# Performance work log

Hardware: AMD Instinct MI355X
Metric: run time of the kernel (lower is better)

The kernel has to match this reference:

```python
import jax, jax.numpy as jnp
import numpy as np

BN_EPS = 1e-5

def _bn_eval(x, gamma, beta):
    # Fresh torch BatchNorm1d in eval mode: running_mean=0, running_var=1
    return x * (gamma / jnp.sqrt(1.0 + BN_EPS)) + beta

def setup_inputs() -> dict:
    key = jax.random.key(0)
    ks = jax.random.split(key, 10)
    Q, K, H, W, D = 64, 128, 24, 8, 128
    L = H * W            # seq_len = 192
    FF = 2048            # dim_feedforward
    q_feat = jax.random.normal(ks[0], (Q, H, W, D), dtype=jnp.float32)
    g_feat = jax.random.normal(ks[1], (K, H, W, D), dtype=jnp.float32)
    se = jax.random.normal(ks[2], (L, L), dtype=jnp.float32)
    score_embed = (se + se.T).reshape(1, 1, L, L)
    s = 1.0 / np.sqrt(D)
    fc0_w = jax.random.uniform(ks[3], (D, D), jnp.float32, -s, s)
    fc0_b = jax.random.uniform(ks[4], (D,), jnp.float32, -s, s)
    s2 = 1.0 / np.sqrt(L)
    fc2_w = jax.random.uniform(ks[5], (FF, L), jnp.float32, -s2, s2)
    fc2_b = jax.random.uniform(ks[6], (FF,), jnp.float32, -s2, s2)
    s3 = 1.0 / np.sqrt(FF)
    fc3_w = jax.random.uniform(ks[7], (1, FF), jnp.float32, -s3, s3)
    fc3_b = jax.random.uniform(ks[8], (1,), jnp.float32, -s3, s3)
    bn1_g = jnp.ones((1,)); bn1_b = jnp.zeros((1,))
    bn2_g = jnp.ones((FF,)) + 0.1 * jax.random.normal(ks[9], (FF,), jnp.float32)
    bn2_b = jnp.zeros((FF,))
    bn3_g = jnp.ones((1,)); bn3_b = jnp.zeros((1,))
    return dict(q_feat=q_feat, g_feat=g_feat, score_embed=score_embed,
                fc0_w=fc0_w, fc0_b=fc0_b, fc2_w=fc2_w, fc2_b=fc2_b,
                fc3_w=fc3_w, fc3_b=fc3_b, bn1_g=bn1_g, bn1_b=bn1_b,
                bn2_g=bn2_g, bn2_b=bn2_b, bn3_g=bn3_g, bn3_b=bn3_b)

def reference(q_feat, g_feat, score_embed, fc0_w, fc0_b, fc2_w, fc2_b,
              fc3_w, fc3_b, bn1_g, bn1_b, bn2_g, bn2_b, bn3_g, bn3_b):
    Q = q_feat.shape[0]
    K = g_feat.shape[0]
    D = q_feat.shape[-1]
    L = score_embed.shape[-1]  # seq_len
    tgt = q_feat.reshape(Q, L, D)
    mem = g_feat.reshape(K, L, D)
    query = tgt @ fc0_w.T + fc0_b      # [Q, L, D]
    key_ = mem @ fc0_w.T + fc0_b       # [K, L, D]
    # [Q, K, L(s), L(t)] score, modulated by broadcast sigmoid bias
    score = jnp.einsum('qtd,ksd->qkst', query, key_) * jax.nn.sigmoid(score_embed)
    score = score.reshape(Q * K, L, L)
    # max over s and over t, concatenated per pair -> [QK, 2L]
    score = jnp.concatenate([score.max(axis=1), score.max(axis=2)], axis=-1)
    score = score.reshape(-1, L)       # [2*QK, L]
    score = _bn_eval(score, bn1_g, bn1_b)
    score = score @ fc2_w.T + fc2_b    # [2*QK, FF]
    score = _bn_eval(score, bn2_g, bn2_b)
    score = jax.nn.relu(score)
    score = score @ fc3_w.T + fc3_b    # [2*QK, 1]
    score = score.reshape(-1, 2).sum(axis=-1, keepdims=True)  # [QK, 1]
    score = _bn_eval(score, bn3_g, bn3_b)
    return score.reshape(Q, K)
```

## Files before the change

kernel.cpp:

```cpp
#include <hip/hip_runtime.h>
#include <hip/hip_fp16.h>

#define LL 192
#define FF 2048

typedef __attribute__((__ext_vector_type__(8)))  __bf16 bf16x8;
typedef __attribute__((__ext_vector_type__(4)))  __bf16 bf16x4;
typedef __attribute__((__ext_vector_type__(4)))  float  f32x4;
typedef __attribute__((__ext_vector_type__(2)))  _Float16 f16x2;

#define MFMA16(a, b, c) __builtin_amdgcn_mfma_f32_16x16x32_bf16((a), (b), (c), 0, 0, 0)


#define ASYNC_LDS16(g, l)                                        \
    __builtin_amdgcn_global_load_lds(                            \
        (const __attribute__((address_space(1))) void*)(g),      \
        (__attribute__((address_space(3))) void*)(l), 16, 0, 0)

template<int CTL>
__device__ __forceinline__ unsigned dppu(unsigned x) {
    return (unsigned)__builtin_amdgcn_mov_dpp((int)x, CTL, 0xF, 0xF, true);
}
__device__ __forceinline__ unsigned pkrtz_u(float a, float b) {
    return __builtin_bit_cast(unsigned, __builtin_amdgcn_cvt_pkrtz(a, b));
}
__device__ __forceinline__ unsigned hmax2u(unsigned a, unsigned b) {
    unsigned r;
    asm("v_pk_max_f16 %0, %1, %2" : "=v"(r) : "v"(a), "v"(b));
    return r;
}

__launch_bounds__(256, 2)
__global__ void proj_prep_kernel(const float* __restrict__ qf_in,
                                 const float* __restrict__ gf_in,
                                 const float* __restrict__ fc0w,
                                 const float* __restrict__ fc0b,
                                 const float* __restrict__ se,
                                 const float* __restrict__ fc2w,
                                 const float* __restrict__ fc2b,
                                 const float* __restrict__ bn2g,
                                 const float* __restrict__ bn2b,
                                 const float* __restrict__ fc3w,
                                 __bf16* __restrict__ kfragA,
                                 __bf16* __restrict__ qfrag16,
                                 float* __restrict__ sig32,
                                 __bf16* __restrict__ fc2w_bf,
                                 float* __restrict__ h2,
                                 float* __restrict__ bb2,
                                 float* __restrict__ f3)
{
    int bx = blockIdx.x, tid = threadIdx.x;
    if (bx >= 1152) {
        int i0 = (bx - 1152) * 256 + tid;
        const int stride = 160 * 256;
        const float c1 = rsqrtf(1.f + 1e-5f);
        for (int i = i0; i < LL * LL; i += stride) {
            int r = i & 3, lane = (i >> 2) & 63, tile = i >> 8;
            int jt = tile % 12, st = tile / 12;
            int s = st * 16 + (lane >> 4) * 4 + r;
            int t = jt * 16 + (lane & 15);
            sig32[i] = 1.f / (1.f + __expf(-se[s * 192 + t]));
        }
        for (int i = i0; i < FF * LL; i += stride)
            fc2w_bf[i] = (__bf16)fc2w[i];
        for (int i = i0; i < FF; i += stride) {
            float h = bn2g[i] * c1;
            h2[i]  = h;
            bb2[i] = fc2b[i] * h + bn2b[i];
            f3[i]  = fc3w[i];
        }
        return;
    }
    __shared__ __bf16 Xs[32][136];
    __shared__ __bf16 Ws[128][136];
    __shared__ __bf16 Os[4096];
    const float* src = (bx < 384) ? (qf_in + (size_t)bx * (32 * 128))
                                  : (gf_in + (size_t)(bx - 384) * (32 * 128));
#pragma unroll
    for (int it = 0; it < 4; ++it) {
        int e = (it * 256 + tid) * 4;
        int r = e >> 7, c = e & 127;
        float4 v = *reinterpret_cast<const float4*>(src + e);
        bf16x4 xv;
        xv[0] = (__bf16)v.x; xv[1] = (__bf16)v.y;
        xv[2] = (__bf16)v.z; xv[3] = (__bf16)v.w;
        *reinterpret_cast<bf16x4*>(&Xs[r][c]) = xv;
    }
#pragma unroll
    for (int it = 0; it < 16; ++it) {
        int e = (it * 256 + tid) * 4;
        int r = e >> 7, c = e & 127;
        float4 v = *reinterpret_cast<const float4*>(fc0w + e);
        bf16x4 xv;
        xv[0] = (__bf16)v.x; xv[1] = (__bf16)v.y;
        xv[2] = (__bf16)v.z; xv[3] = (__bf16)v.w;
        *reinterpret_cast<bf16x4*>(&Ws[r][c]) = xv;
    }
    __syncthreads();

    int wv = tid >> 6, lane = tid & 63, quad = lane >> 4, l16 = lane & 15;
    int n0 = wv * 32;
    f32x4 acc[2][2];
#pragma unroll
    for (int m = 0; m < 2; ++m)
#pragma unroll
        for (int n = 0; n < 2; ++n) acc[m][n] = (f32x4){0.f, 0.f, 0.f, 0.f};
#pragma unroll
    for (int ks = 0; ks < 4; ++ks) {
        bf16x8 a0 = *reinterpret_cast<const bf16x8*>(&Xs[l16][ks * 32 + quad * 8]);
        bf16x8 a1 = *reinterpret_cast<const bf16x8*>(&Xs[16 + l16][ks * 32 + quad * 8]);
        bf16x8 b0 = *reinterpret_cast<const bf16x8*>(&Ws[n0 + l16][ks * 32 + quad * 8]);
        bf16x8 b1 = *reinterpret_cast<const bf16x8*>(&Ws[n0 + 16 + l16][ks * 32 + quad * 8]);
        acc[0][0] = MFMA16(a0, b0, acc[0][0]);
        acc[0][1] = MFMA16(a0, b1, acc[0][1]);
        acc[1][0] = MFMA16(a1, b0, acc[1][0]);
        acc[1][1] = MFMA16(a1, b1, acc[1][1]);
    }
#pragma unroll
    for (int mt = 0; mt < 2; ++mt)
#pragma unroll
        for (int nt = 0; nt < 2; ++nt) {
            int d = n0 + nt * 16 + l16;
            float bv = fc0b[d];
            int abase = mt * 2048 + (d >> 5) * 512 + ((d >> 3) & 3) * 128 + (d & 7);
#pragma unroll
            for (int r = 0; r < 4; ++r)
                Os[abase + (quad * 4 + r) * 8] = (__bf16)(acc[mt][nt][r] + bv);
        }
    __syncthreads();

    int row0 = bx * 32;
    __bf16* dst;
    if (bx < 384) {
        int qi = row0 / 192, tg0 = (row0 % 192) >> 4;
        dst = qfrag16 + qi * 24576 + tg0 * 2048;
    } else {
        int rk0 = row0 - 12288;
        int ki = rk0 / 192, sg0 = (rk0 % 192) >> 4;
        dst = kfragA + ki * 24576 + sg0 * 2048;
    }
#pragma unroll
    for (int it = 0; it < 2; ++it) {
        int e = (it * 256 + tid) * 8;
        *reinterpret_cast<bf16x8*>(dst + e) =
            *reinterpret_cast<const bf16x8*>(&Os[e]);
    }
}

__launch_bounds__(256, 1)
__global__ void score_kernel(const __bf16* __restrict__ kfragA,
                             const __bf16* __restrict__ qfrag16,
                             const float* __restrict__ sig32,
                             const float* __restrict__ bn1g,
                             const float* __restrict__ bn1b,
                             __bf16* __restrict__ Sred)
{
    __shared__ __bf16 Abuf[8192];
    __shared__ unsigned rowP[2][16][98];

    int tid = threadIdx.x;
    int q0 = (blockIdx.x & 31) * 2;
    int kbase = (blockIdx.x >> 5) << 2;
    int w = tid >> 6, lane = tid & 63, quad = lane >> 4, l16 = lane & 15;
    const float g1c = bn1g[0] * rsqrtf(1.f + 1e-5f);
    const float b1v = bn1b[0];

    bf16x8 Bf[2][3][4];
#pragma unroll
    for (int p = 0; p < 2; ++p) {
        const __bf16* qb = qfrag16 + (size_t)(q0 + p) * 24576 + lane * 8;
#pragma unroll
        for (int j = 0; j < 3; ++j)
#pragma unroll
            for (int ks = 0; ks < 4; ++ks)
                Bf[p][j][ks] = *reinterpret_cast<const bf16x8*>(
                    qb + ((3 * w + j) * 4 + ks) * 512);
    }

#pragma unroll 1
    for (int kk = 0; kk < 4; ++kk) {
        int kidx = kbase + kk;
        const __bf16* kp = kfragA + (size_t)kidx * 24576;
        float cm[2][3];
#pragma unroll
        for (int p = 0; p < 2; ++p)
#pragma unroll
            for (int j = 0; j < 3; ++j) cm[p][j] = -3.0e38f;

#pragma unroll 1
        for (int h = 0; h < 3; ++h) {
#pragma unroll
            for (int it = 0; it < 4; ++it)
                ASYNC_LDS16(kp + 8192 * h + (it * 256 + tid) * 8,
                            &Abuf[(it * 256 + (tid & 192)) * 8]);
            __syncthreads();

#pragma unroll
            for (int lsc = 0; lsc < 2; ++lsc) {
                f32x4 acc[2][2][3];
#pragma unroll
                for (int p = 0; p < 2; ++p)
#pragma unroll
                    for (int i = 0; i < 2; ++i)
#pragma unroll
                        for (int j = 0; j < 3; ++j)
                            acc[p][i][j] = (f32x4){0.f, 0.f, 0.f, 0.f};

#pragma unroll
                for (int ks = 0; ks < 4; ++ks) {
                    bf16x8 a0 = *reinterpret_cast<const bf16x8*>(
                        &Abuf[((lsc * 2 + 0) * 4 + ks) * 512 + lane * 8]);
                    bf16x8 a1 = *reinterpret_cast<const bf16x8*>(
                        &Abuf[((lsc * 2 + 1) * 4 + ks) * 512 + lane * 8]);
#pragma unroll
                    for (int j = 0; j < 3; ++j) {
                        acc[0][0][j] = MFMA16(a0, Bf[0][j][ks], acc[0][0][j]);
                        acc[0][1][j] = MFMA16(a1, Bf[0][j][ks], acc[0][1][j]);
                        acc[1][0][j] = MFMA16(a0, Bf[1][j][ks], acc[1][0][j]);
                        acc[1][1][j] = MFMA16(a1, Bf[1][j][ks], acc[1][1][j]);
                    }
                }

#pragma unroll
                for (int i = 0; i < 2; ++i) {
                    int stile = 4 * h + lsc * 2 + i;
                    const float* sp = sig32 +
                        ((size_t)(stile * 12 + 3 * w) * 64 + lane) * 4;
                    f32x4 s0 = *reinterpret_cast<const f32x4*>(sp);
                    f32x4 s1 = *reinterpret_cast<const f32x4*>(sp + 256);
                    f32x4 s2 = *reinterpret_cast<const f32x4*>(sp + 512);
#pragma unroll
                    for (int p = 0; p < 2; ++p) {
                        f32x4 v0 = acc[p][i][0] * s0;
                        f32x4 v1 = acc[p][i][1] * s1;
                        f32x4 v2 = acc[p][i][2] * s2;
                        cm[p][0] = fmaxf(fmaxf(cm[p][0], fmaxf(v0[0], v0[1])),
                                         fmaxf(v0[2], v0[3]));
                        cm[p][1] = fmaxf(fmaxf(cm[p][1], fmaxf(v1[0], v1[1])),
                                         fmaxf(v1[2], v1[3]));
                        cm[p][2] = fmaxf(fmaxf(cm[p][2], fmaxf(v2[0], v2[1])),
                                         fmaxf(v2[2], v2[3]));
                        unsigned h01 = pkrtz_u(
                            fmaxf(fmaxf(v0[0], v1[0]), v2[0]),
                            fmaxf(fmaxf(v0[1], v1[1]), v2[1]));
                        unsigned h23 = pkrtz_u(
                            fmaxf(fmaxf(v0[2], v1[2]), v2[2]),
                            fmaxf(fmaxf(v0[3], v1[3]), v2[3]));
                        h01 = hmax2u(h01, dppu<0xB1>(h01));
                        h01 = hmax2u(h01, dppu<0x4E>(h01));
                        h23 = hmax2u(h23, dppu<0xB1>(h23));
                        h23 = hmax2u(h23, dppu<0x4E>(h23));
                        if ((l16 & 3) == 0) {
                            int rp = stile * 8 + quad * 2;
                            rowP[p][(l16 >> 2) * 4 + w][rp]     = h01;
                            rowP[p][(l16 >> 2) * 4 + w][rp + 1] = h23;
                        }
                    }
                }
            }
            __syncthreads();
        }

#pragma unroll
        for (int p = 0; p < 2; ++p) {
            size_t ob = (size_t)((q0 + p) * 128 + kidx) * 384;
            float v0 = cm[p][0], v1 = cm[p][1], v2 = cm[p][2];
            v0 = fmaxf(v0, __shfl_xor(v0, 16, 64));
            v0 = fmaxf(v0, __shfl_xor(v0, 32, 64));
            v1 = fmaxf(v1, __shfl_xor(v1, 16, 64));
            v1 = fmaxf(v1, __shfl_xor(v1, 32, 64));
            v2 = fmaxf(v2, __shfl_xor(v2, 16, 64));
            v2 = fmaxf(v2, __shfl_xor(v2, 32, 64));
            if (quad == 0) {
                Sred[ob + (3 * w + 0) * 16 + l16] = (__bf16)(v0 * g1c + b1v);
                Sred[ob + (3 * w + 1) * 16 + l16] = (__bf16)(v1 * g1c + b1v);
                Sred[ob + (3 * w + 2) * 16 + l16] = (__bf16)(v2 * g1c + b1v);
            }
        }

        if (tid < 96) {
#pragma unroll
            for (int p = 0; p < 2; ++p) {
                size_t ob = (size_t)((q0 + p) * 128 + kidx) * 384;
                unsigned m = rowP[p][0][tid];
#pragma unroll
                for (int c = 1; c < 16; ++c)
                    m = hmax2u(m, rowP[p][c][tid]);
                __half2 hm = __builtin_bit_cast(__half2, m);
                float lo = __low2float(hm), hi = __high2float(hm);
                unsigned two =
                    (unsigned)__builtin_bit_cast(unsigned short,
                        (__bf16)(lo * g1c + b1v)) |
                    ((unsigned)__builtin_bit_cast(unsigned short,
                        (__bf16)(hi * g1c + b1v)) << 16);
                *reinterpret_cast<unsigned*>(&Sred[ob + 192 + 2 * tid]) = two;
            }
        }
    }
}

__launch_bounds__(512, 1)
__global__ void mlp_kernel(const __bf16* __restrict__ Sred,
                           const __bf16* __restrict__ fc2w_bf,
                           const float* __restrict__ h2,
                           const float* __restrict__ bb2,
                           const float* __restrict__ f3,
                           const float* __restrict__ fc3b,
                           const float* __restrict__ bn3g,
                           const float* __restrict__ bn3b,
                           float* __restrict__ out)
{
    __shared__ __bf16 As[64][200];
    __shared__ float  psum_lds[8][64];
    int bx = blockIdx.x, tid = threadIdx.x;
    const __bf16* asrc = Sred + (size_t)bx * (64 * 192);
#pragma unroll
    for (int it = 0; it < 3; ++it) {
        int e = (it * 512 + tid) * 8;
        int r = e / 192, c = e - r * 192;
        *reinterpret_cast<bf16x8*>(&As[r][c]) =
            *reinterpret_cast<const bf16x8*>(asrc + e);
    }
    __syncthreads();

    int wv = tid >> 6, lane = tid & 63, quad = lane >> 4, l16 = lane & 15;
    bf16x8 af[4][6];
#pragma unroll
    for (int m = 0; m < 4; ++m)
#pragma unroll
        for (int kk = 0; kk < 6; ++kk)
            af[m][kk] = *reinterpret_cast<const bf16x8*>(
                &As[m * 16 + l16][kk * 32 + quad * 8]);

    float ps[4][4] = {{0.f,0.f,0.f,0.f},{0.f,0.f,0.f,0.f},
                      {0.f,0.f,0.f,0.f},{0.f,0.f,0.f,0.f}};
    for (int nt = 0; nt < 16; ++nt) {
        int n0 = wv * 256 + nt * 16;
        f32x4 acc[4];
#pragma unroll
        for (int m = 0; m < 4; ++m) acc[m] = (f32x4){0.f, 0.f, 0.f, 0.f};
        const __bf16* bp = fc2w_bf + (size_t)(n0 + l16) * 192 + quad * 8;
#pragma unroll
        for (int kk = 0; kk < 6; ++kk) {
            bf16x8 b = *reinterpret_cast<const bf16x8*>(bp + kk * 32);
#pragma unroll
            for (int m = 0; m < 4; ++m) acc[m] = MFMA16(af[m][kk], b, acc[m]);
        }
        int n = n0 + l16;
        float hh = h2[n], bb = bb2[n], ffv = f3[n];
#pragma unroll
        for (int m = 0; m < 4; ++m)
#pragma unroll
            for (int r = 0; r < 4; ++r)
                ps[m][r] += fmaxf(acc[m][r] * hh + bb, 0.f) * ffv;
    }
#pragma unroll
    for (int m = 0; m < 4; ++m)
#pragma unroll
        for (int r = 0; r < 4; ++r) {
            float v = ps[m][r];
            v += __shfl_xor(v, 1, 64);
            v += __shfl_xor(v, 2, 64);
            v += __shfl_xor(v, 4, 64);
            v += __shfl_xor(v, 8, 64);
            if (l16 == 0) psum_lds[wv][m * 16 + quad * 4 + r] = v;
        }
    __syncthreads();
    if (tid < 32) {
        float s = 0.f;
#pragma unroll
        for (int w = 0; w < 8; ++w)
            s += psum_lds[w][2 * tid] + psum_lds[w][2 * tid + 1];
        const float c1 = rsqrtf(1.f + 1e-5f);
        out[bx * 32 + tid] = (s + 2.f * fc3b[0]) * (bn3g[0] * c1) + bn3b[0];
    }
}

extern "C" void kernel_launch(void* const* d_in, const int* in_sizes, int n_in,
                              void* d_out, int out_size, void* d_ws, size_t ws_size,
                              hipStream_t stream)
{
    const float* q_feat = (const float*)d_in[0];
    const float* g_feat = (const float*)d_in[1];
    const float* se     = (const float*)d_in[2];
    const float* fc0w   = (const float*)d_in[3];
    const float* fc0b   = (const float*)d_in[4];
    const float* fc2w   = (const float*)d_in[5];
    const float* fc2b   = (const float*)d_in[6];
    const float* fc3w   = (const float*)d_in[7];
    const float* fc3b   = (const float*)d_in[8];
    const float* bn1g   = (const float*)d_in[9];
    const float* bn1b   = (const float*)d_in[10];
    const float* bn2g   = (const float*)d_in[11];
    const float* bn2b   = (const float*)d_in[12];
    const float* bn3g   = (const float*)d_in[13];
    const float* bn3b   = (const float*)d_in[14];
    float* out = (float*)d_out;

    char* ws = (char*)d_ws;
    __bf16* kfragA   = (__bf16*)(ws);
    __bf16* qfrag16  = (__bf16*)(ws +  6291456);
    float*  sig32    = (float*) (ws +  9437184);
    __bf16* fc2w_bf  = (__bf16*)(ws +  9584640);
    float*  h2       = (float*) (ws + 10371072);
    float*  bb2      = (float*) (ws + 10379264);
    float*  f3       = (float*) (ws + 10387456);
    __bf16* Sred     = (__bf16*)(ws + 10395648);

    proj_prep_kernel<<<1312, 256, 0, stream>>>(q_feat, g_feat, fc0w, fc0b, se,
                                               fc2w, fc2b, bn2g, bn2b, fc3w,
                                               kfragA, qfrag16, sig32, fc2w_bf,
                                               h2, bb2, f3);
    score_kernel<<<1024, 256, 0, stream>>>(kfragA, qfrag16, sig32, bn1g, bn1b, Sred);
    mlp_kernel<<<256, 512, 0, stream>>>(Sred, fc2w_bf, h2, bb2, f3,
                                        fc3b, bn3g, bn3b, out);
}
```

Before: 267.0 us.

## Register-prefetch next K tile instead of async global-to-LDS loads

Replaces the direct global_load_lds async copies with a register prefetch: the next 8192-element chunk of K fragments is loaded into registers right after the barrier, so the load overlaps the MFMA work on the current chunk, and is then written to LDS at the top of the next iteration. It also seeds the first MFMA of each accumulator with a zero constant instead of zero-initialising accumulators first. This costs extra VGPRs for the prefetch buffer and a separate LDS store pass, and relies on the existing barrier pattern, which may leave a write-after-read hazard on the single LDS buffer.

```diff
diff --git a/kernel.cpp b/kernel.cpp
--- a/kernel.cpp
+++ b/kernel.cpp
@@ -11,11 +11,6 @@
 
 #define MFMA16(a, b, c) __builtin_amdgcn_mfma_f32_16x16x32_bf16((a), (b), (c), 0, 0, 0)
 
-
-#define ASYNC_LDS16(g, l)                                        \
-    __builtin_amdgcn_global_load_lds(                            \
-        (const __attribute__((address_space(1))) void*)(g),      \
-        (__attribute__((address_space(3))) void*)(l), 16, 0, 0)
 
 template<int CTL>
 __device__ __forceinline__ unsigned dppu(unsigned x) {
@@ -164,6 +159,13 @@
     int w = tid >> 6, lane = tid & 63, quad = lane >> 4, l16 = lane & 15;
     const float g1c = bn1g[0] * rsqrtf(1.f + 1e-5f);
     const float b1v = bn1b[0];
+    const f32x4 Z4 = (f32x4){0.f, 0.f, 0.f, 0.f};
+
+    bf16x8 P[4];
+#pragma unroll
+    for (int it = 0; it < 4; ++it)
+        P[it] = *reinterpret_cast<const bf16x8*>(
+            kfragA + (size_t)kbase * 24576 + (it * 256 + tid) * 8);
 
     bf16x8 Bf[2][3][4];
 #pragma unroll
@@ -180,7 +182,6 @@
 #pragma unroll 1
     for (int kk = 0; kk < 4; ++kk) {
         int kidx = kbase + kk;
-        const __bf16* kp = kfragA + (size_t)kidx * 24576;
         float cm[2][3];
 #pragma unroll
         for (int p = 0; p < 2; ++p)
@@ -191,20 +192,22 @@
         for (int h = 0; h < 3; ++h) {
 #pragma unroll
             for (int it = 0; it < 4; ++it)
-                ASYNC_LDS16(kp + 8192 * h + (it * 256 + tid) * 8,
-                            &Abuf[(it * 256 + (tid & 192)) * 8]);
+                *reinterpret_cast<bf16x8*>(&Abuf[(it * 256 + tid) * 8]) = P[it];
             __syncthreads();
+
+            if (!(kk == 3 && h == 2)) {
+                const __bf16* np = (h < 2)
+                    ? kfragA + (size_t)kidx * 24576 + 8192 * (h + 1)
+                    : kfragA + (size_t)(kidx + 1) * 24576;
+#pragma unroll
+                for (int it = 0; it < 4; ++it)
+                    P[it] = *reinterpret_cast<const bf16x8*>(
+                        np + (it * 256 + tid) * 8);
+            }
 
 #pragma unroll
             for (int lsc = 0; lsc < 2; ++lsc) {
                 f32x4 acc[2][2][3];
-#pragma unroll
-                for (int p = 0; p < 2; ++p)
-#pragma unroll
-                    for (int i = 0; i < 2; ++i)
-#pragma unroll
-                        for (int j = 0; j < 3; ++j)
-                            acc[p][i][j] = (f32x4){0.f, 0.f, 0.f, 0.f};
 
 #pragma unroll
                 for (int ks = 0; ks < 4; ++ks) {
@@ -212,12 +215,22 @@
                         &Abuf[((lsc * 2 + 0) * 4 + ks) * 512 + lane * 8]);
                     bf16x8 a1 = *reinterpret_cast<const bf16x8*>(
                         &Abuf[((lsc * 2 + 1) * 4 + ks) * 512 + lane * 8]);
-#pragma unroll
-                    for (int j = 0; j < 3; ++j) {
-                        acc[0][0][j] = MFMA16(a0, Bf[0][j][ks], acc[0][0][j]);
-                        acc[0][1][j] = MFMA16(a1, Bf[0][j][ks], acc[0][1][j]);
-                        acc[1][0][j] = MFMA16(a0, Bf[1][j][ks], acc[1][0][j]);
-                        acc[1][1][j] = MFMA16(a1, Bf[1][j][ks], acc[1][1][j]);
+                    if (ks == 0) {
+#pragma unroll
+                        for (int j = 0; j < 3; ++j) {
+                            acc[0][0][j] = MFMA16(a0, Bf[0][j][0], Z4);
+                            acc[0][1][j] = MFMA16(a1, Bf[0][j][0], Z4);
+                            acc[1][0][j] = MFMA16(a0, Bf[1][j][0], Z4);
+                            acc[1][1][j] = MFMA16(a1, Bf[1][j][0], Z4);
+                        }
+                    } else {
+#pragma unroll
+                        for (int j = 0; j < 3; ++j) {
+                            acc[0][0][j] = MFMA16(a0, Bf[0][j][ks], acc[0][0][j]);
+                            acc[0][1][j] = MFMA16(a1, Bf[0][j][ks], acc[0][1][j]);
+                            acc[1][0][j] = MFMA16(a0, Bf[1][j][ks], acc[1][0][j]);
+                            acc[1][1][j] = MFMA16(a1, Bf[1][j][ks], acc[1][1][j]);
+                        }
                     }
                 }
 
```

After: 252.0 us. 5.6% less time.
